# Kernel tuning notes

Hardware: AMD Instinct MI355X
Metric: run time of the kernel (lower is better)

## Reference

```python
import jax, jax.numpy as jnp
import numpy as np

H = 64
VOCAB = 64
NUM_PAIRS = 6
ENERGY_THRESHOLD = 0.4
LN_EPS = 1e-5


def setup_inputs() -> dict:
    key = jax.random.key(0)
    ks = jax.random.split(key, 16)
    B, L = 256, 2048
    s = 0.05
    return {
        "x": jax.random.randint(ks[0], (B, L), 0, VOCAB),
        "embed": jax.random.normal(ks[1], (VOCAB, H), jnp.float32) * s,
        "W1": jax.random.normal(ks[2], (2 * H, H), jnp.float32) * s,
        "b1": jnp.zeros((2 * H,), jnp.float32),
        "W2": jax.random.normal(ks[3], (H, 2 * H), jnp.float32) * s,
        "b2": jnp.zeros((H,), jnp.float32),
        "ln_g": jnp.ones((H,), jnp.float32),
        "ln_b": jnp.zeros((H,), jnp.float32),
        "Wk": jax.random.normal(ks[4], (H, H), jnp.float32) * s,
        "Wv": jax.random.normal(ks[5], (H, H), jnp.float32) * s,
        "Wq": jax.random.normal(ks[6], (H, H), jnp.float32) * s,
        "Wr": jax.random.normal(ks[7], (H, H), jnp.float32) * s,
        "alpha": jnp.float32(0.5),
        "Wout": jax.random.normal(ks[8], (VOCAB, H), jnp.float32) * s,
        "bout": jnp.zeros((VOCAB,), jnp.float32),
    }


def _layernorm(x, g, b):
    mu = jnp.mean(x, axis=-1, keepdims=True)
    var = jnp.var(x, axis=-1, keepdims=True)
    return (x - mu) * jax.lax.rsqrt(var + LN_EPS) * g + b


def _encoder(x, embed, W1, b1, W2, b2, ln_g, ln_b):
    h = embed[x]                                  # [B, L, H]
    ff = jax.nn.relu(h @ W1.T + b1) @ W2.T + b2   # [B, L, H]
    return _layernorm(h + ff, ln_g, ln_b)


def _forward(x, embed, W1, b1, W2, b2, ln_g, ln_b, Wk, Wv, Wq, Wr, alpha, Wout, bout):
    h = _encoder(x, embed, W1, b1, W2, b2, ln_g, ln_b)  # [B, L, H]
    B, L, _ = h.shape

    def step(M, h_t):  # M: [B, H, H], h_t: [B, H]
        k = h_t @ Wk.T
        k = k / jnp.maximum(jnp.linalg.norm(k, axis=-1, keepdims=True), 1e-12)
        v = h_t @ Wv.T
        pred = jnp.einsum("bij,bj->bi", M, k)
        delta = v - pred
        gate = (jnp.linalg.norm(delta, axis=-1) >
                ENERGY_THRESHOLD * jnp.linalg.norm(v, axis=-1)).astype(M.dtype)
        M = M + gate[:, None, None] * delta[:, :, None] * k[:, None, :]
        return M, None

    M0 = jnp.zeros((B, H, H), h.dtype)
    M, _ = jax.lax.scan(step, M0, jnp.swapaxes(h, 0, 1))  # scan over L

    q = h[:, -1, :] @ Wq.T                 # [B, H]
    slots = jnp.swapaxes(M, 1, 2)          # [B, H, H]
    k_s = min(NUM_PAIRS + 2, H)
    norms = jnp.linalg.norm(slots, axis=-1)            # [B, H]
    _, topk_i = jax.lax.top_k(norms, k_s)              # [B, k_s]
    sel = jnp.take_along_axis(slots, topk_i[:, :, None], axis=1)  # [B, k_s, H]
    q_r = q @ Wr.T
    attn = jax.nn.softmax(jnp.einsum("bkh,bh->bk", sel, q_r) / jnp.sqrt(jnp.float32(H)), axis=-1)
    retro_ctx = jnp.einsum("bk,bkh->bh", attn, sel)    # [B, H]
    m_ctx = jnp.einsum("bij,bj->bi", M, q)             # [B, H]
    a = jax.nn.sigmoid(alpha)
    mixed = jax.nn.relu(a * retro_ctx + (1.0 - a) * m_ctx)
    return mixed @ Wout.T + bout           # [B, VOCAB]


def reference(x, embed, W1, b1, W2, b2, ln_g, ln_b, Wk, Wv, Wq, Wr, alpha, Wout, bout):
    return _forward(x, embed, W1, b1, W2, b2, ln_g, ln_b, Wk, Wv, Wq, Wr, alpha, Wout, bout)
```

## Files before the change

### kernel.cpp

```cpp
#include <hip/hip_runtime.h>
#include <math.h>

#define H 64
#define VOCABN 64
#define LSEQ 2048
#define LN_EPS 1e-5f

template <int CTRL>
__device__ __forceinline__ float dpp_add(float x) {
  return x + __int_as_float(__builtin_amdgcn_update_dpp(
      0, __float_as_int(x), CTRL, 0xF, 0xF, true));
}

__device__ __forceinline__ float wave_allsum(float x) {
  x = dpp_add<0xB1>(x);
  x = dpp_add<0x4E>(x);
  x = dpp_add<0x141>(x);
  x = dpp_add<0x140>(x);
  x += __shfl_xor(x, 16, 64);
  x += __shfl_xor(x, 32, 64);
  return x;
}

__device__ __forceinline__ float reduce_to_lane63(float x) {
  x = dpp_add<0x111>(x);
  x = dpp_add<0x112>(x);
  x = dpp_add<0x114>(x);
  x = dpp_add<0x118>(x);
  x = dpp_add<0x142>(x);
  x = dpp_add<0x143>(x);
  return x;
}

__global__ __launch_bounds__(64) void tables_kernel(
    const float* __restrict__ embed, const float* __restrict__ W1, const float* __restrict__ b1,
    const float* __restrict__ W2, const float* __restrict__ b2,
    const float* __restrict__ ln_g, const float* __restrict__ ln_b,
    const float* __restrict__ Wk, const float* __restrict__ Wv,
    float* __restrict__ Htab, float* __restrict__ Ktab, float* __restrict__ Vtab,
    float* __restrict__ nvtab)
{
  __shared__ float hs[H];
  __shared__ float ff1[2 * H];
  __shared__ float lns[H];
  const int c = blockIdx.x;
  const int i = threadIdx.x;

  float e = embed[c * H + i];
  hs[i] = e;
  __syncthreads();

  float r1 = b1[i], r2 = b1[i + H];
  for (int j = 0; j < H; ++j) {
    float hj = hs[j];
    r1 = fmaf(W1[i * H + j], hj, r1);
    r2 = fmaf(W1[(i + H) * H + j], hj, r2);
  }
  ff1[i]     = fmaxf(r1, 0.f);
  ff1[i + H] = fmaxf(r2, 0.f);
  __syncthreads();

  float o = b2[i];
  for (int m = 0; m < 2 * H; ++m) o = fmaf(W2[i * 2 * H + m], ff1[m], o);
  float y = e + o;

  float mu  = wave_allsum(y) * (1.f / H);
  float d   = y - mu;
  float var = wave_allsum(d * d) * (1.f / H);
  float ln  = d * (1.f / sqrtf(var + LN_EPS)) * ln_g[i] + ln_b[i];
  lns[i] = ln;
  __syncthreads();
  Htab[c * H + i] = ln;

  float k = 0.f, v = 0.f;
  for (int j = 0; j < H; ++j) {
    float lj = lns[j];
    k = fmaf(Wk[i * H + j], lj, k);
    v = fmaf(Wv[i * H + j], lj, v);
  }
  float nk = sqrtf(wave_allsum(k * k));
  Ktab[c * H + i] = k / fmaxf(nk, 1e-12f);
  Vtab[c * H + i] = v;
  float nv = sqrtf(wave_allsum(v * v));
  if (i == 0) nvtab[c] = 0.4f * nv;
}

__global__ __launch_bounds__(256, 1) void scan_kernel(
    const int* __restrict__ x, const float* __restrict__ Htab,
    const float* __restrict__ Ktab, const float* __restrict__ Vtab,
    const float* __restrict__ nvtab,
    const float* __restrict__ Wq, const float* __restrict__ Wr,
    const float* __restrict__ alpha, const float* __restrict__ Wout,
    const float* __restrict__ bout, float* __restrict__ out)
{
  __shared__ float4 Kl4[VOCABN * H / 4];
  __shared__ float4 Vl4[VOCABN * H / 4];
  __shared__ float4 Gl4[VOCABN * H / 4];
  __shared__ float4 Rl4[VOCABN * H / 4];
  __shared__ int4   xl4[LSEQ / 4];
  __shared__ float  thl[VOCABN];
  __shared__ float  hbuf[H];
  __shared__ float  qbuf[H];
  __shared__ float  mbuf[H];
  float* Kl = (float*)Kl4;
  float* Vl = (float*)Vl4;
  float* Gl = (float*)Gl4;
  float* Rl = (float*)Rl4;
  int*   xl = (int*)xl4;

  const int b    = blockIdx.x;
  const int tid  = threadIdx.x;
  const int lane = tid & 63;
  const int wid  = tid >> 6;

  {
    const float4* Kg = (const float4*)Ktab;
    const float4* Vg = (const float4*)Vtab;
    for (int q = tid; q < VOCABN * H / 4; q += 256) {
      float4 vq = Vg[q];
      Kl4[q] = Kg[q]; Vl4[q] = vq; Rl4[q] = vq;
    }
    const int4* xg = (const int4*)(x + b * LSEQ);
    for (int q = tid; q < LSEQ / 4; q += 256) xl4[q] = xg[q];
    if (tid < VOCABN) thl[tid] = nvtab[tid];
  }
  __syncthreads();

  {
    float4 kr[16];
#pragma unroll
    for (int q = 0; q < 16; ++q) kr[q] = Kl4[lane * 16 + q];
    for (int r = 0; r < 16; ++r) {
      const int c2 = wid * 16 + r;
      const float4* kp2 = (const float4*)(Kl + c2 * H);
      float a0 = 0.f, a1 = 0.f, a2 = 0.f, a3 = 0.f;
#pragma unroll
      for (int q = 0; q < 16; ++q) {
        float4 kq = kp2[q];
        a0 = fmaf(kr[q].x, kq.x, a0);
        a1 = fmaf(kr[q].y, kq.y, a1);
        a2 = fmaf(kr[q].z, kq.z, a2);
        a3 = fmaf(kr[q].w, kq.w, a3);
      }
      Gl[c2 * H + lane] = (a0 + a1) + (a2 + a3);
    }
  }
  __syncthreads();

  float4 M4[16];
#pragma unroll
  for (int q = 0; q < 16; ++q) M4[q] = make_float4(0.f, 0.f, 0.f, 0.f);

  int   c   = xl[0];
  int   cn  = xl[1];
  float rv  = Rl[c * H + lane];
  float thr = thl[c];

  for (int t = 0; t < LSEQ; ++t) {
    float rvn  = Rl[cn * H + lane];
    float thrn = thl[cn];
    const int cn2 = (t + 2 < LSEQ) ? xl[t + 2] : 0;

    float nd2 = reduce_to_lane63(rv * rv);
    float nds = sqrtf(__int_as_float(__builtin_amdgcn_readlane(__float_as_int(nd2), 63)));
    float thu = __int_as_float(__builtin_amdgcn_readfirstlane(__float_as_int(thr)));

    if (nds > thu) {
      __syncthreads();
      const float delta = rv;
#pragma unroll
      for (int r = 0; r < 16; ++r) {
        const int cc = wid * 16 + r;
        float g = Gl[c * H + cc];
        Rl[cc * H + lane] = fmaf(-g, delta, Rl[cc * H + lane]);
      }
      const float4* kp = (const float4*)(Kl + c * H);
#pragma unroll
      for (int q = 0; q < 16; ++q) {
        float4 k4 = kp[q];
        M4[q].x = fmaf(delta, k4.x, M4[q].x);
        M4[q].y = fmaf(delta, k4.y, M4[q].y);
        M4[q].z = fmaf(delta, k4.z, M4[q].z);
        M4[q].w = fmaf(delta, k4.w, M4[q].w);
      }
      __syncthreads();
      rvn = Rl[cn * H + lane];
    }
    rv = rvn; thr = thrn; c = cn; cn = cn2;
  }

  __syncthreads();
  if (wid == 0) {
    float4* MN = (float4*)(Kl + lane * H);
#pragma unroll
    for (int q = 0; q < 16; ++q) MN[q] = M4[q];
#pragma unroll
    for (int q = 0; q < 16; ++q) {
      Vl[(4 * q + 0) * H + lane] = M4[q].x;
      Vl[(4 * q + 1) * H + lane] = M4[q].y;
      Vl[(4 * q + 2) * H + lane] = M4[q].z;
      Vl[(4 * q + 3) * H + lane] = M4[q].w;
    }

    const int clast = xl[LSEQ - 1];
    hbuf[lane] = Htab[clast * H + lane];

    float qi = 0.f;
    for (int j = 0; j < H; ++j) qi = fmaf(Wq[lane * H + j], hbuf[j], qi);
    qbuf[lane] = qi;

    float qri = 0.f;
    for (int j = 0; j < H; ++j) qri = fmaf(Wr[lane * H + j], qbuf[j], qri);

    float n2 = 0.f;
    for (int i2 = 0; i2 < H; ++i2) { float m = Kl[i2 * H + lane]; n2 = fmaf(m, m, n2); }

    const int KS = 8;
    int idxs[KS];
    float nloc = n2;
#pragma unroll
    for (int k = 0; k < KS; ++k) {
      float v = nloc; int idx = lane;
#pragma unroll
      for (int s = 1; s < 64; s <<= 1) {
        float ov = __shfl_xor(v, s, 64);
        int   oi = __shfl_xor(idx, s, 64);
        if (ov > v || (ov == v && oi < idx)) { v = ov; idx = oi; }
      }
      idxs[k] = idx;
      if (lane == idx) nloc = -1.f;
    }

    float sel[KS], lg[KS];
#pragma unroll
    for (int k = 0; k < KS; ++k) {
      float s = Vl[idxs[k] * H + lane];
      sel[k] = s;
      lg[k] = wave_allsum(s * qri) * 0.125f;
    }
    float lmax = lg[0];
#pragma unroll
    for (int k = 1; k < KS; ++k) lmax = fmaxf(lmax, lg[k]);
    float esum = 0.f, retro = 0.f;
#pragma unroll
    for (int k = 0; k < KS; ++k) {
      float e = expf(lg[k] - lmax);
      esum += e;
      retro = fmaf(e, sel[k], retro);
    }
    retro /= esum;

    float mc = 0.f;
#pragma unroll
    for (int q2 = 0; q2 < 16; ++q2) {
      mc = fmaf(M4[q2].x, qbuf[4 * q2 + 0], mc);
      mc = fmaf(M4[q2].y, qbuf[4 * q2 + 1], mc);
      mc = fmaf(M4[q2].z, qbuf[4 * q2 + 2], mc);
      mc = fmaf(M4[q2].w, qbuf[4 * q2 + 3], mc);
    }

    float a = 1.f / (1.f + expf(-alpha[0]));
    float mixed = fmaxf(fmaf(a, retro, (1.f - a) * mc), 0.f);
    mbuf[lane] = mixed;

    float oo = bout[lane];
    for (int i2 = 0; i2 < H; ++i2) oo = fmaf(Wout[lane * H + i2], mbuf[i2], oo);
    out[b * VOCABN + lane] = oo;
  }
}

extern "C" void kernel_launch(void* const* d_in, const int* in_sizes, int n_in,
                              void* d_out, int out_size, void* d_ws, size_t ws_size,
                              hipStream_t stream) {
  const int*   x     = (const int*)d_in[0];
  const float* embed = (const float*)d_in[1];
  const float* W1    = (const float*)d_in[2];
  const float* b1    = (const float*)d_in[3];
  const float* W2    = (const float*)d_in[4];
  const float* b2    = (const float*)d_in[5];
  const float* ln_g  = (const float*)d_in[6];
  const float* ln_b  = (const float*)d_in[7];
  const float* Wk    = (const float*)d_in[8];
  const float* Wv    = (const float*)d_in[9];
  const float* Wq    = (const float*)d_in[10];
  const float* Wr    = (const float*)d_in[11];
  const float* alpha = (const float*)d_in[12];
  const float* Wout  = (const float*)d_in[13];
  const float* bout  = (const float*)d_in[14];
  float* out = (float*)d_out;

  const int B = in_sizes[0] / LSEQ;

  float* ws    = (float*)d_ws;
  float* Htab  = ws;
  float* Ktab  = ws + 4096;
  float* Vtab  = ws + 8192;
  float* nvtab = ws + 12288;

  tables_kernel<<<VOCABN, 64, 0, stream>>>(embed, W1, b1, W2, b2, ln_g, ln_b,
                                           Wk, Wv, Htab, Ktab, Vtab, nvtab);
  scan_kernel<<<B, 256, 0, stream>>>(x, Htab, Ktab, Vtab, nvtab,
                                     Wq, Wr, alpha, Wout, bout, out);
}
```

Before: 655.5 us.

## Batch residual-table updates over eight gated steps to cut block barriers

Gated rank-1 updates are no longer applied to the shared residual table every time they fire. Up to eight deltas and their token ids are kept in registers, and the current residual is rebuilt each step with a short FMA correction chain. The table is flushed with two barriers only once eight updates have accumulated. Only wave 0 now accumulates the M state, which removes redundant work in the other waves but adds register pressure and per-step Gl gather loads.

Result: slower. 869.8 us (+32.7%).

```diff
diff --git a/kernel.cpp b/kernel.cpp
--- a/kernel.cpp
+++ b/kernel.cpp
@@ -151,42 +151,88 @@
 #pragma unroll
   for (int q = 0; q < 16; ++q) M4[q] = make_float4(0.f, 0.f, 0.f, 0.f);
 
+  int   p = 0;
+  float d0 = 0.f, d1 = 0.f, d2 = 0.f, d3 = 0.f, d4 = 0.f, d5 = 0.f, d6 = 0.f, d7 = 0.f;
+  int   s0 = 0,   s1 = 0,   s2 = 0,   s3 = 0,   s4 = 0,   s5 = 0,   s6 = 0,   s7 = 0;
+  float g0 = 0.f, g1 = 0.f, g2 = 0.f, g3 = 0.f, g4 = 0.f, g5 = 0.f, g6 = 0.f, g7 = 0.f;
+
   int   c   = xl[0];
-  int   cn  = xl[1];
-  float rv  = Rl[c * H + lane];
   float thr = thl[c];
+  float rvb = Rl[c * H + lane];
 
   for (int t = 0; t < LSEQ; ++t) {
-    float rvn  = Rl[cn * H + lane];
-    float thrn = thl[cn];
-    const int cn2 = (t + 2 < LSEQ) ? xl[t + 2] : 0;
+    const int cn   = (t + 1 < LSEQ) ? xl[t + 1] : 0;
+    const float thrn = thl[cn];
+
+    float rv = rvb;
+    if (p > 0) {
+      rv = fmaf(-g0, d0, rv); rv = fmaf(-g1, d1, rv);
+      rv = fmaf(-g2, d2, rv); rv = fmaf(-g3, d3, rv);
+      if (p > 4) {
+        rv = fmaf(-g4, d4, rv); rv = fmaf(-g5, d5, rv);
+        rv = fmaf(-g6, d6, rv); rv = fmaf(-g7, d7, rv);
+      }
+    }
 
     float nd2 = reduce_to_lane63(rv * rv);
     float nds = sqrtf(__int_as_float(__builtin_amdgcn_readlane(__float_as_int(nd2), 63)));
     float thu = __int_as_float(__builtin_amdgcn_readfirstlane(__float_as_int(thr)));
 
     if (nds > thu) {
-      __syncthreads();
-      const float delta = rv;
-#pragma unroll
-      for (int r = 0; r < 16; ++r) {
-        const int cc = wid * 16 + r;
-        float g = Gl[c * H + cc];
-        Rl[cc * H + lane] = fmaf(-g, delta, Rl[cc * H + lane]);
-      }
-      const float4* kp = (const float4*)(Kl + c * H);
-#pragma unroll
-      for (int q = 0; q < 16; ++q) {
-        float4 k4 = kp[q];
-        M4[q].x = fmaf(delta, k4.x, M4[q].x);
-        M4[q].y = fmaf(delta, k4.y, M4[q].y);
-        M4[q].z = fmaf(delta, k4.z, M4[q].z);
-        M4[q].w = fmaf(delta, k4.w, M4[q].w);
-      }
-      __syncthreads();
-      rvn = Rl[cn * H + lane];
-    }
-    rv = rvn; thr = thrn; c = cn; cn = cn2;
+      if      (p == 0) { d0 = rv; s0 = c; }
+      else if (p == 1) { d1 = rv; s1 = c; }
+      else if (p == 2) { d2 = rv; s2 = c; }
+      else if (p == 3) { d3 = rv; s3 = c; }
+      else if (p == 4) { d4 = rv; s4 = c; }
+      else if (p == 5) { d5 = rv; s5 = c; }
+      else if (p == 6) { d6 = rv; s6 = c; }
+      else             { d7 = rv; s7 = c; }
+      ++p;
+
+      if (wid == 0) {
+        const float4* kp = (const float4*)(Kl + c * H);
+#pragma unroll
+        for (int q = 0; q < 16; ++q) {
+          float4 k4 = kp[q];
+          M4[q].x = fmaf(rv, k4.x, M4[q].x);
+          M4[q].y = fmaf(rv, k4.y, M4[q].y);
+          M4[q].z = fmaf(rv, k4.z, M4[q].z);
+          M4[q].w = fmaf(rv, k4.w, M4[q].w);
+        }
+      }
+
+      if (p == 8) {
+        __syncthreads();
+#pragma unroll
+        for (int r = 0; r < 16; ++r) {
+          const int cc = wid * 16 + r;
+          float val = Rl[cc * H + lane];
+          val = fmaf(-Gl[s0 * H + cc], d0, val);
+          val = fmaf(-Gl[s1 * H + cc], d1, val);
+          val = fmaf(-Gl[s2 * H + cc], d2, val);
+          val = fmaf(-Gl[s3 * H + cc], d3, val);
+          val = fmaf(-Gl[s4 * H + cc], d4, val);
+          val = fmaf(-Gl[s5 * H + cc], d5, val);
+          val = fmaf(-Gl[s6 * H + cc], d6, val);
+          val = fmaf(-Gl[s7 * H + cc], d7, val);
+          Rl[cc * H + lane] = val;
+        }
+        __syncthreads();
+        d0 = d1 = d2 = d3 = d4 = d5 = d6 = d7 = 0.f;
+        p = 0;
+      }
+    }
+
+    rvb = Rl[cn * H + lane];
+    if (p > 0) {
+      g0 = Gl[s0 * H + cn]; g1 = Gl[s1 * H + cn];
+      g2 = Gl[s2 * H + cn]; g3 = Gl[s3 * H + cn];
+      if (p > 4) {
+        g4 = Gl[s4 * H + cn]; g5 = Gl[s5 * H + cn];
+        g6 = Gl[s6 * H + cn]; g7 = Gl[s7 * H + cn];
+      }
+    }
+    c = cn; thr = thrn;
   }
 
   __syncthreads();
```

## Split M accumulation across waves and forward-correct prefetched residuals in registers

Applied to the files above, without the earlier changes.

Each wave now holds only a 16-column slice of the memory matrix M instead of every wave keeping a full redundant copy, which cuts per-update FMA work and register pressure. The residuals for the next two tokens are prefetched and patched in registers using Gram entries, so the reload of Rl after the second barrier is no longer needed. Gram row values are read as float4 vectors. In exchange, the final M must be gathered through shared memory with an extra barrier, and m_ctx is computed from LDS.

Result: faster. 561.9 us (-14.3%).

```diff
diff --git a/kernel.cpp b/kernel.cpp
--- a/kernel.cpp
+++ b/kernel.cpp
@@ -147,61 +147,72 @@
   }
   __syncthreads();
 
-  float4 M4[16];
-#pragma unroll
-  for (int q = 0; q < 16; ++q) M4[q] = make_float4(0.f, 0.f, 0.f, 0.f);
-
-  int   c   = xl[0];
-  int   cn  = xl[1];
-  float rv  = Rl[c * H + lane];
-  float thr = thl[c];
+  float4 Mw[4];
+#pragma unroll
+  for (int q = 0; q < 4; ++q) Mw[q] = make_float4(0.f, 0.f, 0.f, 0.f);
+
+  int   c0 = xl[0], c1 = xl[1];
+  float rv  = Rl[c0 * H + lane];
+  float rvn = Rl[c1 * H + lane];
+  float th0 = thl[c0], th1 = thl[c1];
 
   for (int t = 0; t < LSEQ; ++t) {
-    float rvn  = Rl[cn * H + lane];
-    float thrn = thl[cn];
-    const int cn2 = (t + 2 < LSEQ) ? xl[t + 2] : 0;
+    const int ix2 = (t + 2 < LSEQ) ? t + 2 : LSEQ - 1;
+    const int c2  = xl[ix2];
+    float rb2  = Rl[c2 * H + lane];
+    float th2v = thl[c2];
+    float g01  = Gl[c0 * H + c1];
+    float g02  = Gl[c0 * H + c2];
 
     float nd2 = reduce_to_lane63(rv * rv);
     float nds = sqrtf(__int_as_float(__builtin_amdgcn_readlane(__float_as_int(nd2), 63)));
-    float thu = __int_as_float(__builtin_amdgcn_readfirstlane(__float_as_int(thr)));
+    float thu = __int_as_float(__builtin_amdgcn_readfirstlane(__float_as_int(th0)));
 
     if (nds > thu) {
+      const float delta = rv;
+      rvn = fmaf(-g01, delta, rvn);
+      rb2 = fmaf(-g02, delta, rb2);
       __syncthreads();
-      const float delta = rv;
+      const float4* gp = ((const float4*)(Gl + c0 * H)) + wid * 4;
+      float4 ga = gp[0], gb = gp[1], gc = gp[2], gd = gp[3];
+      float gs[16] = {ga.x, ga.y, ga.z, ga.w, gb.x, gb.y, gb.z, gb.w,
+                      gc.x, gc.y, gc.z, gc.w, gd.x, gd.y, gd.z, gd.w};
 #pragma unroll
       for (int r = 0; r < 16; ++r) {
         const int cc = wid * 16 + r;
-        float g = Gl[c * H + cc];
-        Rl[cc * H + lane] = fmaf(-g, delta, Rl[cc * H + lane]);
+        Rl[cc * H + lane] = fmaf(-gs[r], delta, Rl[cc * H + lane]);
       }
-      const float4* kp = (const float4*)(Kl + c * H);
-#pragma unroll
-      for (int q = 0; q < 16; ++q) {
+      const float4* kp = ((const float4*)(Kl + c0 * H)) + wid * 4;
+#pragma unroll
+      for (int q = 0; q < 4; ++q) {
         float4 k4 = kp[q];
-        M4[q].x = fmaf(delta, k4.x, M4[q].x);
-        M4[q].y = fmaf(delta, k4.y, M4[q].y);
-        M4[q].z = fmaf(delta, k4.z, M4[q].z);
-        M4[q].w = fmaf(delta, k4.w, M4[q].w);
+        Mw[q].x = fmaf(delta, k4.x, Mw[q].x);
+        Mw[q].y = fmaf(delta, k4.y, Mw[q].y);
+        Mw[q].z = fmaf(delta, k4.z, Mw[q].z);
+        Mw[q].w = fmaf(delta, k4.w, Mw[q].w);
       }
       __syncthreads();
-      rvn = Rl[cn * H + lane];
-    }
-    rv = rvn; thr = thrn; c = cn; cn = cn2;
-  }
-
-  __syncthreads();
+    }
+    rv = rvn; rvn = rb2; c0 = c1; c1 = c2; th0 = th1; th1 = th2v;
+  }
+
+  __syncthreads();
+#pragma unroll
+  for (int r = 0; r < 4; ++r) {
+    const int jb = wid * 16 + r * 4;
+    float4 m = Mw[r];
+    Vl[(jb + 0) * H + lane] = m.x;
+    Vl[(jb + 1) * H + lane] = m.y;
+    Vl[(jb + 2) * H + lane] = m.z;
+    Vl[(jb + 3) * H + lane] = m.w;
+    Kl[lane * H + jb + 0] = m.x;
+    Kl[lane * H + jb + 1] = m.y;
+    Kl[lane * H + jb + 2] = m.z;
+    Kl[lane * H + jb + 3] = m.w;
+  }
+  __syncthreads();
+
   if (wid == 0) {
-    float4* MN = (float4*)(Kl + lane * H);
-#pragma unroll
-    for (int q = 0; q < 16; ++q) MN[q] = M4[q];
-#pragma unroll
-    for (int q = 0; q < 16; ++q) {
-      Vl[(4 * q + 0) * H + lane] = M4[q].x;
-      Vl[(4 * q + 1) * H + lane] = M4[q].y;
-      Vl[(4 * q + 2) * H + lane] = M4[q].z;
-      Vl[(4 * q + 3) * H + lane] = M4[q].w;
-    }
-
     const int clast = xl[LSEQ - 1];
     hbuf[lane] = Htab[clast * H + lane];
 
@@ -251,13 +262,7 @@
     retro /= esum;
 
     float mc = 0.f;
-#pragma unroll
-    for (int q2 = 0; q2 < 16; ++q2) {
-      mc = fmaf(M4[q2].x, qbuf[4 * q2 + 0], mc);
-      mc = fmaf(M4[q2].y, qbuf[4 * q2 + 1], mc);
-      mc = fmaf(M4[q2].z, qbuf[4 * q2 + 2], mc);
-      mc = fmaf(M4[q2].w, qbuf[4 * q2 + 3], mc);
-    }
+    for (int j = 0; j < H; ++j) mc = fmaf(Vl[j * H + lane], qbuf[j], mc);
 
     float a = 1.f / (1.f + expf(-alpha[0]));
     float mixed = fmaxf(fmaf(a, retro, (1.f - a) * mc), 0.f);
```
